# Kernel tuning notes

Hardware: AMD Instinct MI355X
Metric: run time of the kernel (lower is better)

Reference implementation:

```python
import jax, jax.numpy as jnp
import numpy as np

H = W = 256      # image_size from __init__
CHUNK = 64       # triangles processed per scan step (bounds peak memory)


def setup_inputs() -> dict:
    key = jax.random.key(0)
    k1, k2, k3, k4, k5 = jax.random.split(key, 5)
    B, V, F = 2, 5023, 2048
    vertices = jax.random.normal(k1, (B, V, 3), jnp.float32)
    # transformed (camera-space / NDC) vertices: x,y in [-1,1], z = depth
    transformed_vertices = jax.random.uniform(k2, (B, V, 3), jnp.float32, -1.0, 1.0)
    textures = jax.random.uniform(k3, (B, 256, 256, 3), jnp.float32)
    uvcoords = jax.random.uniform(k4, (V, 2), jnp.float32)
    faces = jax.random.randint(k5, (F, 3), 0, V, jnp.int32)
    return dict(vertices=vertices, transformed_vertices=transformed_vertices,
                textures=textures, uvcoords=uvcoords, faces=faces)


def _bilinear_sample(tex, uv):
    # tex [Ht,Wt,3], uv [V,2] in [0,1] -> [V,3]
    Ht, Wt = tex.shape[0], tex.shape[1]
    u = uv[:, 0] * (Wt - 1)
    v = uv[:, 1] * (Ht - 1)
    u0 = jnp.clip(jnp.floor(u), 0, Wt - 2).astype(jnp.int32)
    v0 = jnp.clip(jnp.floor(v), 0, Ht - 2).astype(jnp.int32)
    fu = (u - u0)[:, None]
    fv = (v - v0)[:, None]
    c00 = tex[v0, u0]; c01 = tex[v0, u0 + 1]
    c10 = tex[v0 + 1, u0]; c11 = tex[v0 + 1, u0 + 1]
    return (c00 * (1 - fu) + c01 * fu) * (1 - fv) + (c10 * (1 - fu) + c11 * fu) * fv


def _rasterize(tv, faces, h, w):
    # Per-pixel z-buffered rasterization with barycentric weights.
    # tv [B,V,3] in NDC, faces [F,3] -> (zbuf [B,h,w], face_id [B,h,w], bary [B,h,w,3])
    B = tv.shape[0]
    F = faces.shape[0]
    xs = (jnp.arange(w, dtype=jnp.float32) + 0.5) / w * 2.0 - 1.0
    ys = (jnp.arange(h, dtype=jnp.float32) + 0.5) / h * 2.0 - 1.0
    px, py = jnp.meshgrid(xs, ys)                      # [h,w]
    tri = tv[:, faces]                                 # [B,F,3,3] gather
    nchunks = F // CHUNK
    tris = tri.reshape(B, nchunks, CHUNK, 3, 3).transpose(1, 0, 2, 3, 4)
    bases = jnp.arange(nchunks, dtype=jnp.int32) * CHUNK

    def step(carry, xs_):
        zbuf, fid, bary = carry
        t, base = xs_                                  # t [B,C,3,3]
        x0, y0, z0 = t[:, :, 0, 0], t[:, :, 0, 1], t[:, :, 0, 2]
        x1, y1, z1 = t[:, :, 1, 0], t[:, :, 1, 1], t[:, :, 1, 2]
        x2, y2, z2 = t[:, :, 2, 0], t[:, :, 2, 1], t[:, :, 2, 2]
        denom = (y1 - y2) * (x0 - x2) + (x2 - x1) * (y0 - y2)   # [B,C]
        inv = jnp.where(jnp.abs(denom) > 1e-8, 1.0 / jnp.where(jnp.abs(denom) > 1e-8, denom, 1.0), 0.0)
        e = lambda a: a[:, :, None, None]
        w0 = (e(y1 - y2) * (px - e(x2)) + e(x2 - x1) * (py - e(y2))) * e(inv)  # [B,C,h,w]
        w1 = (e(y2 - y0) * (px - e(x2)) + e(x0 - x2) * (py - e(y2))) * e(inv)
        w2 = 1.0 - w0 - w1
        inside = (w0 >= 0) & (w1 >= 0) & (w2 >= 0) & (jnp.abs(denom)[:, :, None, None] > 1e-8)
        z = w0 * e(z0) + w1 * e(z1) + w2 * e(z2)
        zm = jnp.where(inside, z, -jnp.inf)
        bz = jnp.max(zm, axis=1)                       # best z within chunk [B,h,w]
        bi = jnp.argmax(zm, axis=1)
        take = lambda a: jnp.take_along_axis(a, bi[:, None], axis=1)[:, 0]
        bw = jnp.stack([take(w0), take(w1), take(w2)], -1)      # [B,h,w,3]
        upd = bz > zbuf                                # z-buffer test (init -1, larger z = closer)
        zbuf = jnp.where(upd, bz, zbuf)
        fid = jnp.where(upd, base + bi.astype(jnp.int32), fid)
        bary = jnp.where(upd[..., None], bw, bary)
        return (zbuf, fid, bary), None

    init = (jnp.full((B, h, w), -1.0, jnp.float32),
            jnp.full((B, h, w), -1, jnp.int32),
            jnp.zeros((B, h, w, 3), jnp.float32))
    (zbuf, fid, bary), _ = jax.lax.scan(jax.checkpoint(step), init, (tris, bases))
    return zbuf, fid, bary


def reference(vertices, transformed_vertices, textures, uvcoords, faces):
    zbuf, fid, bary = _rasterize(transformed_vertices, faces, H, W)
    # create_attributes: per-vertex attributes = sampled texture color + world position
    vcol = jax.vmap(_bilinear_sample, in_axes=(0, None))(textures, uvcoords)  # [B,V,3]
    vattr = jnp.concatenate([vcol, vertices], axis=-1)                        # [B,V,6]
    fattr = vattr[:, faces]                                                   # [B,F,3,6]
    # interpolate: gather face attributes by face_id, blend with barycentrics
    safe_fid = jnp.maximum(fid, 0)
    pix = jax.vmap(lambda fa, fi: fa[fi])(fattr, safe_fid)                    # [B,h,w,3,6]
    img = jnp.einsum('bhwkc,bhwk->bhwc', pix, bary)
    alpha = (fid >= 0).astype(jnp.float32)
    img = img * alpha[..., None]
    rendered_images = img.transpose(0, 3, 1, 2)       # [B,6,H,W]
    alpha_images = alpha[:, None]                     # [B,1,H,W]
    return rendered_images, alpha_images, fid, zbuf
```

## Files before the change

kernel.cpp:

```cpp
#include <hip/hip_runtime.h>

#define HWD 256
#define NB 2
#define NV 5023
#define NF 2048


__device__ __forceinline__ float pix_coord(int i) {
    return ((float)i + 0.5f) * 0.0078125f - 1.0f;
}

__device__ __forceinline__ int z_bucket(float zmax) {
    int k = (int)((1.0f - zmax) * 128.0f);
    return min(max(k, 0), 255);
}

__global__ __launch_bounds__(256) void k_prep(const float* __restrict__ verts,
                                              const float* __restrict__ tex,
                                              const float* __restrict__ uv,
                                              const float* __restrict__ tv,
                                              const int* __restrict__ faces,
                                              float* __restrict__ frP,
                                              float* __restrict__ vattr,
                                              unsigned long long* __restrict__ zk,
                                              unsigned int* __restrict__ hist) {
    int blk = blockIdx.x, tid = threadIdx.x;
    if (blk < 512) {
        zk[blk * 256 + tid] = (0x407FFFFFull << 32) | 0x80000000ull;
        return;
    }
    if (blk < 552) {
        int i = (blk - 512) * 256 + tid;
        if (i >= NB * NV) return;
        int b = i / NV, v = i - b * NV;
        float u = __fmul_rn(uv[2 * v + 0], 255.0f);
        float w = __fmul_rn(uv[2 * v + 1], 255.0f);
        float uf = floorf(u); uf = fminf(fmaxf(uf, 0.0f), 254.0f);
        float vf = floorf(w); vf = fminf(fmaxf(vf, 0.0f), 254.0f);
        int u0 = (int)uf, v0 = (int)vf;
        float fu = __fsub_rn(u, uf);
        float fv = __fsub_rn(w, vf);
        const float* t   = tex + (size_t)b * HWD * HWD * 3;
        const float* c00 = t + ((size_t)v0 * HWD + u0) * 3;
        const float* c01 = c00 + 3;
        const float* c10 = c00 + HWD * 3;
        const float* c11 = c10 + 3;
        float gu = 1.0f - fu, gv = 1.0f - fv;
        float* o = vattr + (size_t)i * 6;
        for (int c = 0; c < 3; ++c) {
            float l0 = c00[c] * gu + c01[c] * fu;
            float l1 = c10[c] * gu + c11[c] * fu;
            o[c] = l0 * gv + l1 * fv;
        }
        const float* vp = verts + ((size_t)b * NV + v) * 3;
        o[3] = vp[0]; o[4] = vp[1]; o[5] = vp[2];
        return;
    }
    int i = (blk - 552) * 256 + tid;
    if (i >= NB * NF) return;
    int b = i / NF, f = i - b * NF;
    int i0 = faces[3 * f + 0], i1 = faces[3 * f + 1], i2 = faces[3 * f + 2];
    const float* base = tv + (size_t)b * NV * 3;
    float x0 = base[3 * i0 + 0], y0 = base[3 * i0 + 1], z0 = base[3 * i0 + 2];
    float x1 = base[3 * i1 + 0], y1 = base[3 * i1 + 1], z1 = base[3 * i1 + 2];
    float x2 = base[3 * i2 + 0], y2 = base[3 * i2 + 1], z2 = base[3 * i2 + 2];

    float dy12 = __fsub_rn(y1, y2);
    float dx21 = __fsub_rn(x2, x1);
    float dy20 = __fsub_rn(y2, y0);
    float dx02 = __fsub_rn(x0, x2);
    float denom = __fadd_rn(__fmul_rn(dy12, __fsub_rn(x0, x2)),
                            __fmul_rn(dx21, __fsub_rn(y0, y2)));
    bool valid = fabsf(denom) > 1e-8f;

    int xlo = 1, xhi = 0, ylo = 1, yhi = 0;
    if (valid) {
        if (fabsf(denom) < 1e-3f) {
            xlo = 0; xhi = 255; ylo = 0; yhi = 255;
        } else {
            float xmn = fminf(x0, fminf(x1, x2)), xmx = fmaxf(x0, fmaxf(x1, x2));
            float ymn = fminf(y0, fminf(y1, y2)), ymx = fmaxf(y0, fmaxf(y1, y2));
            xlo = (int)floorf((xmn + 1.0f) * 128.0f - 0.5f) - 1;
            xhi = (int)ceilf ((xmx + 1.0f) * 128.0f - 0.5f) + 1;
            ylo = (int)floorf((ymn + 1.0f) * 128.0f - 0.5f) - 1;
            yhi = (int)ceilf ((ymx + 1.0f) * 128.0f - 0.5f) + 1;
            xlo = max(xlo, 0); ylo = max(ylo, 0);
            xhi = min(xhi, 255); yhi = min(yhi, 255);
            if (xhi < xlo || yhi < ylo) { xlo = 1; xhi = 0; ylo = 1; yhi = 0; }
        }
    }
    float zmax = valid ? fmaxf(z0, fmaxf(z1, z2)) : -2.0f;
    float* o = frP + (size_t)i * 16;
    o[0] = dy12; o[1] = dx21; o[2] = x2; o[3] = y2;
    o[4] = dy20; o[5] = dx02; o[6] = valid ? (1.0f / denom) : 0.0f;
    o[7] = z0; o[8] = z1; o[9] = z2;
    ((unsigned int*)o)[10] = (unsigned)xlo | ((unsigned)xhi << 16);
    ((unsigned int*)o)[11] = (unsigned)ylo | ((unsigned)yhi << 16);
    o[12] = denom;
    o[13] = zmax;
    atomicAdd(&hist[b * 256 + z_bucket(zmax)], 1u);
}

__global__ __launch_bounds__(1024) void k_scatter(const float* __restrict__ frP,
                                                  const unsigned int* __restrict__ hist,
                                                  float* __restrict__ rFace) {
    int tid = threadIdx.x;
    __shared__ unsigned int a[512];
    __shared__ unsigned int cur[512];
    unsigned int v = 0;
    if (tid < 512) { v = hist[tid]; a[tid] = v; }
    __syncthreads();
    for (int off = 1; off < 512; off <<= 1) {
        unsigned int t = 0;
        if (tid < 512 && tid >= off) t = a[tid - off];
        __syncthreads();
        if (tid < 512) a[tid] += t;
        __syncthreads();
    }
    if (tid < 512) cur[tid] = a[tid] - v;
    __syncthreads();

    for (int i = tid; i < NB * NF; i += 1024) {
        const float* o = frP + (size_t)i * 16;
        int b = i >> 11, fid = i & (NF - 1);
        float zmax = o[13];
        int k = z_bucket(zmax);
        unsigned int p = atomicAdd(&cur[b * 256 + k], 1u);
        unsigned int rank = p - (unsigned)(b * NF);
        unsigned int slot = (rank & 7u) * 256u + (rank >> 3);
        float* rf = rFace + (((size_t)b * NF + slot) << 4);
        bool skip = fabsf(o[12]) < 1e-3f;
        rf[0] = o[10]; rf[1] = o[11];
        rf[2] = __uint_as_float((unsigned)fid | ((unsigned)skip << 16));
        rf[3] = 1.0f - (float)k * 0.0078125f + 1e-6f;
        rf[4] = o[0]; rf[5] = o[1]; rf[6] = o[2]; rf[7] = o[3];
        rf[8] = o[4]; rf[9] = o[5]; rf[10] = o[6]; rf[11] = o[7];
        rf[12] = o[8]; rf[13] = o[9]; rf[14] = 0.0f; rf[15] = 0.0f;
    }
}

__global__ __launch_bounds__(256) void k_raster(const float* __restrict__ rFace,
                                                unsigned long long* __restrict__ zk) {
    int bid  = blockIdx.x;
    int tile = bid & 255;
    int seg  = (bid >> 8) & 7;
    int b    = bid >> 11;
    int tid = threadIdx.x, wave = tid >> 6, lane = tid & 63;

    __shared__ float fdat[256 * 20];
    __shared__ unsigned int cntw[4];
    __shared__ float redmin[4];

    int tlx = tile & 15, tly = tile >> 4;

    {
        int slot = seg * 256 + tid;
        const float4* src = (const float4*)(rFace + (((size_t)b * NF + slot) << 4));
        float4 h = src[0], g0 = src[1], g1 = src[2], g2 = src[3];
        unsigned int bbx = __float_as_uint(h.x), bby = __float_as_uint(h.y);
        int xlo = (int)(bbx & 0xffffu), xhi = (int)(bbx >> 16);
        int ylo = (int)(bby & 0xffffu), yhi = (int)(bby >> 16);
        int pxlo = tlx << 4, pxhi = pxlo + 15, pylo = tly << 4, pyhi = pylo + 15;
        bool keep = (xhi >= xlo) && (xlo <= pxhi) && (xhi >= pxlo)
                                 && (ylo <= pyhi) && (yhi >= pylo);
        bool skip = (__float_as_uint(h.z) >> 16) != 0u;
        if (keep && !skip) {
            float inv = g1.z, x2 = g0.z, y2 = g0.w;
            float A0 = g0.x * inv, B0 = g0.y * inv;
            float A1 = g1.x * inv, B1 = g1.y * inv;
            float C = A0 + A1, D = B0 + B1;
            float x0n = pix_coord(pxlo), x1n = pix_coord(pxhi);
            float y0n = pix_coord(pylo), y1n = pix_coord(pyhi);
            float w0m = A0 * ((A0 > 0.f ? x1n : x0n) - x2) + B0 * ((B0 > 0.f ? y1n : y0n) - y2);
            float w1m = A1 * ((A1 > 0.f ? x1n : x0n) - x2) + B1 * ((B1 > 0.f ? y1n : y0n) - y2);
            float w2m = 1.0f - (C * ((C > 0.f ? x0n : x1n) - x2) + D * ((D > 0.f ? y0n : y1n) - y2));
            keep = (w0m >= -0.02f) && (w1m >= -0.02f) && (w2m >= -0.02f);
        }
        unsigned long long mask = __ballot(keep);
        if (keep) {
            int pos = __popcll(mask & ((1ull << lane) - 1ull));
            float* dst = &fdat[(size_t)(wave * 64 + pos) * 20];
            ((float4*)dst)[0] = h; ((float4*)dst)[1] = g0;
            ((float4*)dst)[2] = g1; ((float4*)dst)[3] = g2;
        }
        if (lane == 0) cntw[wave] = (unsigned int)__popcll(mask);
    }
    __syncthreads();

    int px = (tlx << 4) + (tid & 15), py = (tly << 4) + (tid >> 4);
    float pxf = pix_coord(px), pyf = pix_coord(py);
    unsigned long long best = 0ull;
    float curz = -1.0f;
    bool done = false;

    for (int w = 0; w < 4 && !done; ++w) {
        int n = (int)cntw[w];
        for (int j = 0; j < n; ++j) {
            if ((j & 15) == 0) {
                float m = curz;
                #pragma unroll
                for (int off = 1; off < 64; off <<= 1) m = fminf(m, __shfl_xor(m, off));
                __syncthreads();
                if (lane == 0) redmin[wave] = m;
                __syncthreads();
                float mb = fminf(fminf(redmin[0], redmin[1]), fminf(redmin[2], redmin[3]));
                float ub = fdat[(size_t)(w * 64 + j) * 20 + 3];
                if (ub < mb - 1e-5f) { done = true; break; }
            }
            const float* fp = &fdat[(size_t)(w * 64 + j) * 20];
            float x2 = fp[6], y2 = fp[7];
            float t0 = __fsub_rn(pxf, x2);
            float t1 = __fsub_rn(pyf, y2);
            float w0 = __fmul_rn(__fadd_rn(__fmul_rn(fp[4], t0), __fmul_rn(fp[5], t1)), fp[10]);
            float w1 = __fmul_rn(__fadd_rn(__fmul_rn(fp[8], t0), __fmul_rn(fp[9], t1)), fp[10]);
            float w2 = __fsub_rn(__fsub_rn(1.0f, w0), w1);
            if (w0 >= 0.0f && w1 >= 0.0f && w2 >= 0.0f) {
                float z = __fadd_rn(__fadd_rn(__fmul_rn(w0, fp[11]), __fmul_rn(w1, fp[12])),
                                    __fmul_rn(w2, fp[13]));
                unsigned int fid = __float_as_uint(fp[2]) & 0xFFFFu;
                unsigned int ub32 = __float_as_uint(z);
                unsigned int hi = ub32 ^ ((unsigned int)(((int)ub32) >> 31) | 0x80000000u);
                unsigned long long key = ((unsigned long long)hi << 32)
                                       | (unsigned long long)(0x7FFFFFFFu - fid);
                if (key > best) { best = key; curz = z; }
            }
        }
    }

    if (best) {
        int pix = (b << 16) + py * HWD + px;
        unsigned long long cur = zk[pix];
        if (best > cur) atomicMax(&zk[pix], best);
    }
}

__global__ __launch_bounds__(256) void k_shade(const unsigned long long* __restrict__ zk,
                                               const float* __restrict__ frP,
                                               const int* __restrict__ faces,
                                               const float* __restrict__ vattr,
                                               float* __restrict__ out) {
    int i = blockIdx.x * 256 + threadIdx.x;
    int b = i >> 16;
    int pix = i & 0xFFFF;
    unsigned long long key = zk[i];
    unsigned int lo = (unsigned int)key;
    unsigned int hi = (unsigned int)(key >> 32);

    float img[6] = {0, 0, 0, 0, 0, 0};
    float alpha, fidf, zout;
    if (lo > 0x7FFFFFFFu) {
        alpha = 0.0f; fidf = -1.0f; zout = -1.0f;
    } else {
        int f = (int)(0x7FFFFFFFu - lo);
        unsigned int zb32 = (hi & 0x80000000u) ? (hi & 0x7FFFFFFFu) : ~hi;
        zout = __uint_as_float(zb32);
        alpha = 1.0f;
        fidf = (float)f;
        const float* fp = frP + ((size_t)(b * NF + f)) * 16;
        int px = pix & 0xFF, py = pix >> 8;
        float t0 = __fsub_rn(pix_coord(px), fp[2]);
        float t1 = __fsub_rn(pix_coord(py), fp[3]);
        float w0 = __fmul_rn(__fadd_rn(__fmul_rn(fp[0], t0), __fmul_rn(fp[1], t1)), fp[6]);
        float w1 = __fmul_rn(__fadd_rn(__fmul_rn(fp[4], t0), __fmul_rn(fp[5], t1)), fp[6]);
        float w2 = __fsub_rn(__fsub_rn(1.0f, w0), w1);
        int i0 = faces[3 * f + 0], i1 = faces[3 * f + 1], i2 = faces[3 * f + 2];
        const float* a0 = vattr + ((size_t)b * NV + i0) * 6;
        const float* a1 = vattr + ((size_t)b * NV + i1) * 6;
        const float* a2 = vattr + ((size_t)b * NV + i2) * 6;
        for (int c = 0; c < 6; ++c)
            img[c] = __fadd_rn(__fadd_rn(__fmul_rn(w0, a0[c]), __fmul_rn(w1, a1[c])),
                               __fmul_rn(w2, a2[c]));
    }

    const size_t plane = (size_t)HWD * HWD;
    for (int c = 0; c < 6; ++c)
        out[((size_t)b * 6 + c) * plane + pix] = img[c];
    out[786432 + i]  = alpha;
    out[917504 + i]  = fidf;
    out[1048576 + i] = zout;
}

extern "C" void kernel_launch(void* const* d_in, const int* in_sizes, int n_in,
                              void* d_out, int out_size, void* d_ws, size_t ws_size,
                              hipStream_t stream) {
    (void)in_sizes; (void)n_in; (void)out_size; (void)ws_size;
    const float* verts = (const float*)d_in[0];
    const float* tv    = (const float*)d_in[1];
    const float* tex   = (const float*)d_in[2];
    const float* uv    = (const float*)d_in[3];
    const int*   faces = (const int*)d_in[4];
    float* out = (float*)d_out;

    char* ws = (char*)d_ws;
    unsigned long long* zk    = (unsigned long long*)ws;
    float*              frP   = (float*)(ws + 0x100000);
    float*              vattr = (float*)(ws + 0x140000);
    float*              rFace = (float*)(ws + 0x180000);
    unsigned int*       hist  = (unsigned int*)(ws + 0x1C0000);

    hipMemsetAsync(hist, 0, 512 * sizeof(unsigned int), stream);
    k_prep   <<<568, 256, 0, stream>>>(verts, tex, uv, tv, faces, frP, vattr, zk, hist);
    k_scatter<<<1, 1024, 0, stream>>>(frP, hist, rFace);
    k_raster <<<NB * 8 * 256, 256, 0, stream>>>(rFace, zk);
    k_shade  <<<512, 256, 0, stream>>>(zk, frP, faces, vattr, out);
}
```

Baseline: 129.6 us.

## Fuse shading into raster via last-block counter and drop memset launch

Fuses the shade kernel into the raster kernel. A per-tile atomic counter lets the last of the 8 segment blocks for a tile shade that tile's pixels, which removes one kernel launch. The z-bucket histogram now lives in shared memory inside the single-block scatter kernel, so the global-atomic histogram and the memset go away, and the done counters are zeroed in the prep kernel instead. The raster loop drops its block-wide min reduction for a per-wave early exit, checked every 8 faces instead of every 16, and reads face data as float4 vectors. In exchange it adds threadfence and acquire-load ordering, and the single-block scatter now does extra serial work.

```diff
diff --git a/kernel.cpp b/kernel.cpp
--- a/kernel.cpp
+++ b/kernel.cpp
@@ -23,14 +23,18 @@
                                               float* __restrict__ frP,
                                               float* __restrict__ vattr,
                                               unsigned long long* __restrict__ zk,
-                                              unsigned int* __restrict__ hist) {
+                                              unsigned int* __restrict__ done) {
     int blk = blockIdx.x, tid = threadIdx.x;
     if (blk < 512) {
         zk[blk * 256 + tid] = (0x407FFFFFull << 32) | 0x80000000ull;
         return;
     }
-    if (blk < 552) {
-        int i = (blk - 512) * 256 + tid;
+    if (blk < 514) {
+        done[(blk - 512) * 256 + tid] = 0;
+        return;
+    }
+    if (blk < 554) {
+        int i = (blk - 514) * 256 + tid;
         if (i >= NB * NV) return;
         int b = i / NV, v = i - b * NV;
         float u = __fmul_rn(uv[2 * v + 0], 255.0f);
@@ -56,7 +60,7 @@
         o[3] = vp[0]; o[4] = vp[1]; o[5] = vp[2];
         return;
     }
-    int i = (blk - 552) * 256 + tid;
+    int i = (blk - 554) * 256 + tid;
     if (i >= NB * NF) return;
     int b = i / NF, f = i - b * NF;
     int i0 = faces[3 * f + 0], i1 = faces[3 * f + 1], i2 = faces[3 * f + 2];
@@ -98,18 +102,22 @@
     ((unsigned int*)o)[11] = (unsigned)ylo | ((unsigned)yhi << 16);
     o[12] = denom;
     o[13] = zmax;
-    atomicAdd(&hist[b * 256 + z_bucket(zmax)], 1u);
 }
 
 __global__ __launch_bounds__(1024) void k_scatter(const float* __restrict__ frP,
-                                                  const unsigned int* __restrict__ hist,
                                                   float* __restrict__ rFace) {
     int tid = threadIdx.x;
     __shared__ unsigned int a[512];
     __shared__ unsigned int cur[512];
-    unsigned int v = 0;
-    if (tid < 512) { v = hist[tid]; a[tid] = v; }
-    __syncthreads();
+    if (tid < 512) a[tid] = 0;
+    __syncthreads();
+    for (int i = tid; i < NB * NF; i += 1024) {
+        float zmax = frP[((size_t)i << 4) + 13];
+        int b = i >> 11;
+        atomicAdd(&a[b * 256 + z_bucket(zmax)], 1u);
+    }
+    __syncthreads();
+    unsigned int v = (tid < 512) ? a[tid] : 0;
     for (int off = 1; off < 512; off <<= 1) {
         unsigned int t = 0;
         if (tid < 512 && tid >= off) t = a[tid - off];
@@ -121,10 +129,9 @@
     __syncthreads();
 
     for (int i = tid; i < NB * NF; i += 1024) {
-        const float* o = frP + (size_t)i * 16;
+        const float* o = frP + ((size_t)i << 4);
         int b = i >> 11, fid = i & (NF - 1);
-        float zmax = o[13];
-        int k = z_bucket(zmax);
+        int k = z_bucket(o[13]);
         unsigned int p = atomicAdd(&cur[b * 256 + k], 1u);
         unsigned int rank = p - (unsigned)(b * NF);
         unsigned int slot = (rank & 7u) * 256u + (rank >> 3);
@@ -140,16 +147,21 @@
 }
 
 __global__ __launch_bounds__(256) void k_raster(const float* __restrict__ rFace,
-                                                unsigned long long* __restrict__ zk) {
+                                                const float* __restrict__ frP,
+                                                const int* __restrict__ faces,
+                                                const float* __restrict__ vattr,
+                                                unsigned long long* __restrict__ zk,
+                                                unsigned int* __restrict__ done,
+                                                float* __restrict__ out) {
     int bid  = blockIdx.x;
     int tile = bid & 255;
     int seg  = (bid >> 8) & 7;
     int b    = bid >> 11;
     int tid = threadIdx.x, wave = tid >> 6, lane = tid & 63;
 
-    __shared__ float fdat[256 * 20];
+    __shared__ __align__(16) float fdat[256 * 20];
     __shared__ unsigned int cntw[4];
-    __shared__ float redmin[4];
+    __shared__ unsigned int lastFlag;
 
     int tlx = tile & 15, tly = tile >> 4;
 
@@ -191,33 +203,30 @@
     float pxf = pix_coord(px), pyf = pix_coord(py);
     unsigned long long best = 0ull;
     float curz = -1.0f;
-    bool done = false;
-
-    for (int w = 0; w < 4 && !done; ++w) {
+    bool wdone = false;
+
+    for (int w = 0; w < 4 && !wdone; ++w) {
         int n = (int)cntw[w];
         for (int j = 0; j < n; ++j) {
-            if ((j & 15) == 0) {
+            int base = (w * 64 + j) * 20;
+            if ((j & 7) == 0) {
                 float m = curz;
                 #pragma unroll
                 for (int off = 1; off < 64; off <<= 1) m = fminf(m, __shfl_xor(m, off));
-                __syncthreads();
-                if (lane == 0) redmin[wave] = m;
-                __syncthreads();
-                float mb = fminf(fminf(redmin[0], redmin[1]), fminf(redmin[2], redmin[3]));
-                float ub = fdat[(size_t)(w * 64 + j) * 20 + 3];
-                if (ub < mb - 1e-5f) { done = true; break; }
+                if (fdat[base + 3] < m - 1e-5f) { wdone = true; break; }
             }
-            const float* fp = &fdat[(size_t)(w * 64 + j) * 20];
-            float x2 = fp[6], y2 = fp[7];
-            float t0 = __fsub_rn(pxf, x2);
-            float t1 = __fsub_rn(pyf, y2);
-            float w0 = __fmul_rn(__fadd_rn(__fmul_rn(fp[4], t0), __fmul_rn(fp[5], t1)), fp[10]);
-            float w1 = __fmul_rn(__fadd_rn(__fmul_rn(fp[8], t0), __fmul_rn(fp[9], t1)), fp[10]);
+            const float4 g0 = *(const float4*)&fdat[base + 4];
+            const float4 g1 = *(const float4*)&fdat[base + 8];
+            const float4 g2 = *(const float4*)&fdat[base + 12];
+            float t0 = __fsub_rn(pxf, g0.z);
+            float t1 = __fsub_rn(pyf, g0.w);
+            float w0 = __fmul_rn(__fadd_rn(__fmul_rn(g0.x, t0), __fmul_rn(g0.y, t1)), g1.z);
+            float w1 = __fmul_rn(__fadd_rn(__fmul_rn(g1.x, t0), __fmul_rn(g1.y, t1)), g1.z);
             float w2 = __fsub_rn(__fsub_rn(1.0f, w0), w1);
             if (w0 >= 0.0f && w1 >= 0.0f && w2 >= 0.0f) {
-                float z = __fadd_rn(__fadd_rn(__fmul_rn(w0, fp[11]), __fmul_rn(w1, fp[12])),
-                                    __fmul_rn(w2, fp[13]));
-                unsigned int fid = __float_as_uint(fp[2]) & 0xFFFFu;
+                float z = __fadd_rn(__fadd_rn(__fmul_rn(w0, g1.w), __fmul_rn(w1, g2.x)),
+                                    __fmul_rn(w2, g2.y));
+                unsigned int fid = __float_as_uint(fdat[base + 2]) & 0xFFFFu;
                 unsigned int ub32 = __float_as_uint(z);
                 unsigned int hi = ub32 ^ ((unsigned int)(((int)ub32) >> 31) | 0x80000000u);
                 unsigned long long key = ((unsigned long long)hi << 32)
@@ -227,22 +236,20 @@
         }
     }
 
+    int pix = (b << 16) + py * HWD + px;
     if (best) {
-        int pix = (b << 16) + py * HWD + px;
         unsigned long long cur = zk[pix];
         if (best > cur) atomicMax(&zk[pix], best);
     }
-}
-
-__global__ __launch_bounds__(256) void k_shade(const unsigned long long* __restrict__ zk,
-                                               const float* __restrict__ frP,
-                                               const int* __restrict__ faces,
-                                               const float* __restrict__ vattr,
-                                               float* __restrict__ out) {
-    int i = blockIdx.x * 256 + threadIdx.x;
-    int b = i >> 16;
-    int pix = i & 0xFFFF;
-    unsigned long long key = zk[i];
+
+    __threadfence();
+    if (tid == 0) lastFlag = atomicAdd(&done[b * 256 + tile], 1u);
+    __syncthreads();
+    if (lastFlag != 7u) return;
+    __threadfence();
+
+    unsigned long long key = __hip_atomic_load(&zk[pix], __ATOMIC_ACQUIRE,
+                                               __HIP_MEMORY_SCOPE_AGENT);
     unsigned int lo = (unsigned int)key;
     unsigned int hi = (unsigned int)(key >> 32);
 
@@ -256,10 +263,9 @@
         zout = __uint_as_float(zb32);
         alpha = 1.0f;
         fidf = (float)f;
-        const float* fp = frP + ((size_t)(b * NF + f)) * 16;
-        int px = pix & 0xFF, py = pix >> 8;
-        float t0 = __fsub_rn(pix_coord(px), fp[2]);
-        float t1 = __fsub_rn(pix_coord(py), fp[3]);
+        const float* fp = frP + (((size_t)(b * NF + f)) << 4);
+        float t0 = __fsub_rn(pxf, fp[2]);
+        float t1 = __fsub_rn(pyf, fp[3]);
         float w0 = __fmul_rn(__fadd_rn(__fmul_rn(fp[0], t0), __fmul_rn(fp[1], t1)), fp[6]);
         float w1 = __fmul_rn(__fadd_rn(__fmul_rn(fp[4], t0), __fmul_rn(fp[5], t1)), fp[6]);
         float w2 = __fsub_rn(__fsub_rn(1.0f, w0), w1);
@@ -273,11 +279,12 @@
     }
 
     const size_t plane = (size_t)HWD * HWD;
+    int ppix = py * HWD + px;
     for (int c = 0; c < 6; ++c)
-        out[((size_t)b * 6 + c) * plane + pix] = img[c];
-    out[786432 + i]  = alpha;
-    out[917504 + i]  = fidf;
-    out[1048576 + i] = zout;
+        out[((size_t)b * 6 + c) * plane + ppix] = img[c];
+    out[786432 + pix]  = alpha;
+    out[917504 + pix]  = fidf;
+    out[1048576 + pix] = zout;
 }
 
 extern "C" void kernel_launch(void* const* d_in, const int* in_sizes, int n_in,
@@ -296,11 +303,9 @@
     float*              frP   = (float*)(ws + 0x100000);
     float*              vattr = (float*)(ws + 0x140000);
     float*              rFace = (float*)(ws + 0x180000);
-    unsigned int*       hist  = (unsigned int*)(ws + 0x1C0000);
-
-    hipMemsetAsync(hist, 0, 512 * sizeof(unsigned int), stream);
-    k_prep   <<<568, 256, 0, stream>>>(verts, tex, uv, tv, faces, frP, vattr, zk, hist);
-    k_scatter<<<1, 1024, 0, stream>>>(frP, hist, rFace);
-    k_raster <<<NB * 8 * 256, 256, 0, stream>>>(rFace, zk);
-    k_shade  <<<512, 256, 0, stream>>>(zk, frP, faces, vattr, out);
-}
+    unsigned int*       done  = (unsigned int*)(ws + 0x1C0000);
+
+    k_prep   <<<570, 256, 0, stream>>>(verts, tex, uv, tv, faces, frP, vattr, zk, done);
+    k_scatter<<<1, 1024, 0, stream>>>(frP, rFace);
+    k_raster <<<NB * 8 * 256, 256, 0, stream>>>(rFace, frP, faces, vattr, zk, done, out);
+}
```

After: 411.8 us. 218% more time.
